# Kernel optimization log

Hardware: AMD Instinct MI355X
Metric: run time of the kernel (lower is better)

## Reference

```python
import jax, jax.numpy as jnp
import numpy as np
import math

N_HEADS = 16
D_KV = 64
NUM_BUCKETS = 32
MAX_DISTANCE = 128


def _rel_bucket(rel_pos, num_buckets=NUM_BUCKETS, max_distance=MAX_DISTANCE):
    # bidirectional=True branch of relative_position_bucket
    n = -rel_pos
    num_buckets //= 2
    ret = (n < 0).astype(jnp.int32) * num_buckets
    n = jnp.abs(n)
    max_exact = num_buckets // 2
    is_small = n < max_exact
    val_large = max_exact + (
        jnp.log(n.astype(jnp.float32) / max_exact)
        / math.log(max_distance / max_exact)
        * (num_buckets - max_exact)
    ).astype(jnp.int32)
    val_large = jnp.minimum(val_large, num_buckets - 1)
    return jnp.where(is_small, n, val_large) + ret


def setup_inputs() -> dict:
    key = jax.random.key(0)
    ks = jax.random.split(key, 6)
    T, D = 2048, 1024
    x = jax.random.normal(ks[0], (T, D), dtype=jnp.float32)
    Wq = jax.random.normal(ks[1], (D, N_HEADS * D_KV), dtype=jnp.float32) * 0.02
    Wk = jax.random.normal(ks[2], (D, N_HEADS * D_KV), dtype=jnp.float32) * 0.02
    Wv = jax.random.normal(ks[3], (D, N_HEADS * D_KV), dtype=jnp.float32) * 0.02
    Wo = jax.random.normal(ks[4], (N_HEADS * D_KV, D), dtype=jnp.float32) * 0.02
    rel_bias_table = jax.random.normal(ks[5], (NUM_BUCKETS, N_HEADS), dtype=jnp.float32) * 0.02
    q_lens = jnp.full((4,), 512, dtype=jnp.int32)  # packed varlen: 4 seqs of 512, sum == T
    return {"x": x, "Wq": Wq, "Wk": Wk, "Wv": Wv, "Wo": Wo,
            "rel_bias_table": rel_bias_table, "q_lens": q_lens}


def _attention(x, Wq, Wk, Wv, Wo, rel_bias_table, q_lens):
    T = x.shape[0]
    q = x @ Wq
    k = x @ Wk
    v = x @ Wv
    to_heads = lambda t: jnp.transpose(t.reshape(T, N_HEADS, D_KV), (1, 0, 2))  # [H,T,d]
    q_h, k_h, v_h = to_heads(q), to_heads(k), to_heads(v)

    # fp32 scores (no 1/sqrt(d) scaling in T5; module uses scaling=1.0)
    scores = jnp.einsum('hqd,hkd->hqk', q_h.astype(jnp.float32), k_h.astype(jnp.float32))

    # sequence ids / positions within packed layout
    starts = jnp.cumsum(q_lens, dtype=jnp.int32) - q_lens
    indicators = jnp.zeros(T, dtype=jnp.int32).at[starts].set(1)
    seq_ids = jnp.cumsum(indicators, dtype=jnp.int32) - 1
    pos = jnp.arange(T) - starts[seq_ids]

    # relative position bias (encoder: bidirectional)
    rel_pos = pos[None, :] - pos[:, None]  # [T,T]
    buckets = _rel_bucket(rel_pos)
    bias = jnp.transpose(rel_bias_table[buckets], (2, 0, 1))  # [H,T,T]
    scores = scores + bias.astype(jnp.float32)

    # block-diagonal mask over packed sequences (non-causal encoder)
    total = jnp.sum(q_lens)
    valid = jnp.arange(T) < total
    mask = (seq_ids[:, None] == seq_ids[None, :]) & valid[:, None] & valid[None, :]
    scores = jnp.where(mask[None], scores, jnp.finfo(scores.dtype).min)

    weights = jax.nn.softmax(scores, axis=-1)
    out = jnp.einsum('hqk,hkd->hqd', weights, v_h.astype(jnp.float32))
    out = jnp.transpose(out, (1, 0, 2)).reshape(T, N_HEADS * D_KV)
    return out.astype(x.dtype) @ Wo


def reference(x, Wq, Wk, Wv, Wo, rel_bias_table, q_lens):
    return _attention(x, Wq, Wk, Wv, Wo, rel_bias_table, q_lens)
```

## Files before the change

### kernel.cpp

```cpp
#include <hip/hip_runtime.h>

#define NH 16

typedef __bf16 bf16x8 __attribute__((ext_vector_type(8)));
typedef unsigned short u16x8 __attribute__((ext_vector_type(8)));
typedef float f32x4 __attribute__((ext_vector_type(4)));
typedef unsigned short u16;

__device__ __forceinline__ u16 f2bu(float f) {
    unsigned int u = __builtin_bit_cast(unsigned int, f);
    u = (u + 0x7FFFu + ((u >> 16) & 1u)) >> 16;
    return (u16)u;
}
__device__ __forceinline__ bf16x8 ld_bf8(const u16* p) {
    return __builtin_bit_cast(bf16x8, *(const u16x8*)p);
}
__device__ __forceinline__ void gl_lds16(const void* g, void* l) {
    __builtin_amdgcn_global_load_lds((const __attribute__((address_space(1))) void*)g,
                                     (__attribute__((address_space(3))) void*)l, 16, 0, 0);
}

__device__ __forceinline__ int rel_bucket(int delta) {
    int n = -delta;
    int ret = (n < 0) ? 16 : 0;
    int na = n < 0 ? -n : n;
    int b;
    if (na < 8) b = na;
    else if (na < 12) b = 8;
    else if (na < 16) b = 9;
    else if (na < 23) b = 10;
    else if (na < 32) b = 11;
    else if (na < 46) b = 12;
    else if (na < 64) b = 13;
    else if (na < 91) b = 14;
    else b = 15;
    return b + ret;
}

#define L2E 1.4426950408889634f

__global__ void prep_all(const float* __restrict__ x, u16* __restrict__ xb, int n,
                         const float* __restrict__ tbl, float* __restrict__ biasT, int T,
                         const int* __restrict__ q_lens, int nseq,
                         int* __restrict__ seqid, int* __restrict__ kvs, int* __restrict__ kve,
                         const float* __restrict__ Wq, const float* __restrict__ Wk,
                         const float* __restrict__ Wv, const float* __restrict__ Wo,
                         u16* __restrict__ Wt, u16* __restrict__ Wot,
                         int cb, int bb, int mb) {
    __shared__ float tile[32][33];
    int b = blockIdx.x, tid = threadIdx.x;
    if (b < cb) {
        int i = (b * 256 + tid) * 4;
        if (i >= n) return;
        float4 v = *(const float4*)&x[i];
        u16 o0 = f2bu(v.x), o1 = f2bu(v.y), o2 = f2bu(v.z), o3 = f2bu(v.w);
        xb[i] = o0; xb[i+1] = o1; xb[i+2] = o2; xb[i+3] = o3;
    } else if (b < cb + bb) {
        int idx = (b - cb) * 256 + tid;
        int W = 2 * T - 1;
        if (idx >= NH * W) return;
        int d = idx % W - (T - 1);
        int h = idx / W;
        biasT[idx] = tbl[rel_bucket(d) * NH + h] * L2E;
    } else if (b < cb + bb + mb) {
        int t = (b - cb - bb) * 256 + tid;
        if (t >= T) return;
        int start = 0, sid = -1, a = 0, e = 0;
        for (int i = 0; i < nseq; ++i) {
            int len = q_lens[i];
            if (t >= start && t < start + len) { sid = i; a = start; e = start + len; }
            start += len;
        }
        seqid[t] = sid; kvs[t] = a; kve[t] = e;
    } else {
        int t = b - cb - bb - mb;
        int z = t >> 10; t &= 1023;
        const float* src = z == 0 ? Wq : z == 1 ? Wk : z == 2 ? Wv : Wo;
        u16* dst = z < 3 ? Wt + (size_t)z * 1024 * 1024 : Wot;
        int r0 = (t >> 5) * 32, c0 = (t & 31) * 32;
        int tx = tid & 31, ty = tid >> 5;
        #pragma unroll
        for (int i = 0; i < 32; i += 8)
            tile[ty + i][tx] = src[(size_t)(r0 + ty + i) * 1024 + c0 + tx];
        __syncthreads();
        #pragma unroll
        for (int i = 0; i < 32; i += 8)
            dst[(size_t)(c0 + ty + i) * 1024 + r0 + tx] = f2bu(tile[tx][ty + i]);
    }
}

template<int MODE, int BM>
__global__ __launch_bounds__(256)
void gemm_bt(const u16* __restrict__ A, const u16* __restrict__ Bt,
             int N, int K, int T,
             float* __restrict__ Cf, u16* __restrict__ qkb, u16* __restrict__ vtb) {
    constexpr int MI = BM / 32;
    constexpr int STG = (BM + 128) * 64;
    constexpr int LDSN = (MODE == 1 && 128 * 136 > 2 * STG) ? 128 * 136 : 2 * STG;
    __shared__ __attribute__((aligned(16))) u16 lds[LDSN];
    const int tid = threadIdx.x;
    const int l = tid & 63, wv = tid >> 6;
    const int l16 = l & 15, lg = l >> 4;
    const int lrow = l >> 3, lslot = l & 7;
    const int wm = (wv >> 1) * (BM / 2), wn = (wv & 1) * 64;

    int nbk = gridDim.x * gridDim.y;
    int lin = blockIdx.y * gridDim.x + blockIdx.x;
    int lin2 = (nbk & 7) ? lin : (lin & 7) * (nbk >> 3) + (lin >> 3);
    const int bm = (lin2 % gridDim.x) * BM;
    const int bn = (lin2 / gridDim.x) * 128;

    f32x4 acc[MI][4];
    #pragma unroll
    for (int i = 0; i < MI; i++)
        #pragma unroll
        for (int j = 0; j < 4; j++)
            #pragma unroll
            for (int r = 0; r < 4; r++) acc[i][j][r] = 0.f;

    auto stage = [&](int k0, int bi) {
        u16* As_ = lds + bi * STG;
        u16* Bs_ = As_ + BM * 64;
        #pragma unroll
        for (int c = 0; c < MI; ++c) {
            int chunk = c * 4 + wv;
            int row = chunk * 8 + lrow;
            int gs = lslot ^ (row & 7);
            gl_lds16(&A[(size_t)(bm + row) * K + k0 + gs * 8], &As_[chunk * 512]);
        }
        #pragma unroll
        for (int c = 0; c < 4; ++c) {
            int chunk = c * 4 + wv;
            int row = chunk * 8 + lrow;
            int gs = lslot ^ (row & 7);
            gl_lds16(&Bt[(size_t)(bn + row) * K + k0 + gs * 8], &Bs_[chunk * 512]);
        }
    };

    stage(0, 0);
    __syncthreads();
    int cur = 0;
    for (int k0 = 0; k0 < K; k0 += 64) {
        if (k0 + 64 < K) stage(k0 + 64, cur ^ 1);
        const u16* As = lds + cur * STG;
        const u16* Bs = As + BM * 64;
        #pragma unroll
        for (int kk = 0; kk < 2; ++kk) {
            bf16x8 af[MI], bfv[4];
            #pragma unroll
            for (int i = 0; i < MI; i++) {
                int row = wm + i * 16 + l16;
                af[i] = ld_bf8(&As[row * 64 + (((kk * 4 + lg) ^ (row & 7)) * 8)]);
            }
            #pragma unroll
            for (int j = 0; j < 4; j++) {
                int row = wn + j * 16 + l16;
                bfv[j] = ld_bf8(&Bs[row * 64 + (((kk * 4 + lg) ^ (row & 7)) * 8)]);
            }
            #pragma unroll
            for (int i = 0; i < MI; i++)
                #pragma unroll
                for (int j = 0; j < 4; j++)
                    acc[i][j] = __builtin_amdgcn_mfma_f32_16x16x32_bf16(af[i], bfv[j], acc[i][j], 0, 0, 0);
        }
        __syncthreads();
        cur ^= 1;
    }

    if (MODE == 0) {
        #pragma unroll
        for (int i = 0; i < MI; i++)
            #pragma unroll
            for (int j = 0; j < 4; j++) {
                int col = bn + wn + j * 16 + l16;
                #pragma unroll
                for (int r = 0; r < 4; r++) {
                    int row = bm + wm + i * 16 + lg * 4 + r;
                    Cf[(size_t)row * N + col] = acc[i][j][r];
                }
            }
    } else if (bn < 2048) {
        #pragma unroll
        for (int i = 0; i < MI; i++)
            #pragma unroll
            for (int j = 0; j < 4; j++) {
                int col = bn + wn + j * 16 + l16;
                #pragma unroll
                for (int r = 0; r < 4; r++) {
                    int row = bm + wm + i * 16 + lg * 4 + r;
                    qkb[(size_t)row * 2048 + col] = f2bu(acc[i][j][r]);
                }
            }
    } else {
        #pragma unroll
        for (int i = 0; i < MI; i++)
            #pragma unroll
            for (int j = 0; j < 4; j++) {
                int cl = wn + j * 16 + l16;
                #pragma unroll
                for (int r = 0; r < 4; r++)
                    ((u16*)lds)[cl * 136 + wm + i * 16 + lg * 4 + r] = f2bu(acc[i][j][r]);
            }
        __syncthreads();
        int cl = tid >> 1, hf = tid & 1;
        size_t gb = (size_t)(bn - 2048 + cl) * T + bm + hf * 64;
        #pragma unroll
        for (int k2 = 0; k2 < 8; ++k2) {
            int4 v4 = *(const int4*)&((u16*)lds)[cl * 136 + hf * 64 + k2 * 8];
            *(int4*)&vtb[gb + k2 * 8] = v4;
        }
    }
}

__global__ __launch_bounds__(256)
void attn_kernel(const u16* __restrict__ qkb, const u16* __restrict__ vtb,
                 const float* __restrict__ biasT,
                 const int* __restrict__ seqid, const int* __restrict__ kvsA,
                 const int* __restrict__ kveA,
                 u16* __restrict__ attnb, int T) {
    __shared__ __attribute__((aligned(16))) u16 KV[2][2][4096];
    __shared__ __attribute__((aligned(16))) u16 Ps[4][16][72];
    __shared__ float biasLds[2304];
    const int tid = threadIdx.x;
    const int l = tid & 63, wv = tid >> 6;
    const int l16 = l & 15, lg = l >> 4;
    const int lrow = l >> 3, lslot = l & 7;
    const int Wb = 2 * T - 1;

    int nbk = gridDim.x * gridDim.y;
    int lin = blockIdx.y * gridDim.x + blockIdx.x;
    int lin2 = (nbk & 7) ? lin : (lin & 7) * (nbk >> 3) + (lin >> 3);
    const int h = lin2 / gridDim.x;
    const int q0 = (lin2 % gridDim.x) * 64;

    bf16x8 qf[2];
    {
        int tq = q0 + wv * 16 + l16;
        const u16* qp = qkb + (size_t)tq * 2048 + h * 64 + lg * 8;
        qf[0] = ld_bf8(qp); qf[1] = ld_bf8(qp + 32);
    }
    const int s0 = seqid[q0], s1 = seqid[q0 + 63];
    const bool uni = (s0 == s1) && (s0 >= 0);
    const int kvA = uni ? kvsA[q0] : 0;
    const int kvB = uni ? kveA[q0] : T;
    const int len = kvB - kvA;

    for (int t = tid; t < len + 126; t += 256) {
        int dlt = kvA - q0 + t - 63;
        dlt = dlt < -(T - 1) ? -(T - 1) : (dlt > T - 1 ? T - 1 : dlt);
        biasLds[t] = biasT[(size_t)h * Wb + dlt + (T - 1)];
    }

    const u16* kg = qkb + 1024 + h * 64;
    const u16* vg = vtb + (size_t)(h * 64) * T;

    auto stage = [&](int base, int bi) {
        #pragma unroll
        for (int c = 0; c < 2; ++c) {
            int chunk = c * 4 + wv;
            int row = chunk * 8 + lrow;
            int gs = lslot ^ (row & 7);
            int tk = base + row; if (tk > T - 1) tk = T - 1;
            gl_lds16(kg + (size_t)tk * 2048 + gs * 8, &KV[bi][0][chunk * 512]);
            gl_lds16(vg + (size_t)row * T + base + gs * 8, &KV[bi][1][chunk * 512]);
        }
    };

    int tqr[4], sqr[4];
    #pragma unroll
    for (int r = 0; r < 4; r++) {
        tqr[r] = q0 + wv * 16 + lg * 4 + r;
        sqr[r] = uni ? s0 : seqid[tqr[r]];
    }
    float psum[4] = {0.f, 0.f, 0.f, 0.f};
    f32x4 o[4];
    #pragma unroll
    for (int d = 0; d < 4; d++)
        #pragma unroll
        for (int r = 0; r < 4; r++) o[d][r] = 0.f;

    stage(kvA, 0);
    __syncthreads();
    int cur = 0;
    for (int base = kvA; base < kvB; base += 64) {
        if (base + 64 < kvB) stage(base + 64, cur ^ 1);
        const u16* Kb = KV[cur][0];
        const u16* Vb = KV[cur][1];

        f32x4 s[4];
        #pragma unroll
        for (int kt = 0; kt < 4; kt++)
            #pragma unroll
            for (int r = 0; r < 4; r++) s[kt][r] = 0.f;
        #pragma unroll
        for (int kk = 0; kk < 2; kk++)
            #pragma unroll
            for (int kt = 0; kt < 4; kt++) {
                int r = kt * 16 + l16;
                bf16x8 kf = ld_bf8(Kb + r * 64 + (((kk * 4 + lg) ^ (r & 7)) * 8));
                s[kt] = __builtin_amdgcn_mfma_f32_16x16x32_bf16(qf[kk], kf, s[kt], 0, 0, 0);
            }

        const bool fullT = (base + 64 <= kvB);
        const int cbi = (base - kvA) + 63 + l16 - wv * 16 - lg * 4;
        #pragma unroll
        for (int r = 0; r < 4; r++) {
            const float* bp = &biasLds[cbi - r];
            #pragma unroll
            for (int kt = 0; kt < 4; kt++) {
                float p = __builtin_amdgcn_exp2f(__builtin_fmaf(s[kt][r], L2E, bp[kt * 16]));
                if (uni) {
                    if (!fullT && base + kt * 16 + l16 >= kvB) p = 0.f;
                } else {
                    int tk = base + kt * 16 + l16;
                    int tkc = tk < T ? tk : T - 1;
                    bool ok = (tk < T) && (seqid[tkc] == sqr[r]);
                    p = (sqr[r] < 0) ? 1.f : (ok ? p : 0.f);
                }
                psum[r] += p;
                Ps[wv][lg * 4 + r][kt * 16 + l16] = f2bu(p);
            }
        }
        bf16x8 pf0 = ld_bf8(&Ps[wv][l16][lg * 8]);
        bf16x8 pf1 = ld_bf8(&Ps[wv][l16][32 + lg * 8]);
        #pragma unroll
        for (int kk = 0; kk < 2; kk++) {
            bf16x8 pf = kk ? pf1 : pf0;
            #pragma unroll
            for (int dt = 0; dt < 4; dt++) {
                int r = dt * 16 + l16;
                bf16x8 vf = ld_bf8(Vb + r * 64 + (((kk * 4 + lg) ^ (r & 7)) * 8));
                o[dt] = __builtin_amdgcn_mfma_f32_16x16x32_bf16(pf, vf, o[dt], 0, 0, 0);
            }
        }
        __syncthreads();
        cur ^= 1;
    }

    float lsum[4];
    #pragma unroll
    for (int r = 0; r < 4; r++) {
        float v = psum[r];
        #pragma unroll
        for (int m = 1; m < 16; m <<= 1) v += __shfl_xor(v, m, 64);
        lsum[r] = v;
    }
    #pragma unroll
    for (int dt = 0; dt < 4; dt++)
        #pragma unroll
        for (int r = 0; r < 4; r++)
            attnb[(size_t)tqr[r] * 1024 + h * 64 + dt * 16 + l16] = f2bu(o[dt][r] / lsum[r]);
}

extern "C" void kernel_launch(void* const* d_in, const int* in_sizes, int n_in,
                              void* d_out, int out_size, void* d_ws, size_t ws_size,
                              hipStream_t stream) {
    const float* x   = (const float*)d_in[0];
    const float* Wq  = (const float*)d_in[1];
    const float* Wk  = (const float*)d_in[2];
    const float* Wv  = (const float*)d_in[3];
    const float* Wo  = (const float*)d_in[4];
    const float* tbl = (const float*)d_in[5];
    const int* q_lens = (const int*)d_in[6];
    const int T = in_sizes[0] / 1024;
    const int nseq = in_sizes[6];

    char* ws = (char*)d_ws;
    auto alloc = [&](size_t bytes) { char* p = ws; ws += (bytes + 255) & ~(size_t)255; return p; };
    u16*   xb    = (u16*)alloc((size_t)T * 1024 * 2);
    u16*   Wt    = (u16*)alloc((size_t)3072 * 1024 * 2);
    u16*   Wot   = (u16*)alloc((size_t)1024 * 1024 * 2);
    u16*   qkb   = (u16*)alloc((size_t)T * 2048 * 2);
    u16*   vtb   = (u16*)alloc((size_t)1024 * T * 2);
    u16*   attnb = (u16*)alloc((size_t)T * 1024 * 2);
    float* biasT = (float*)alloc((size_t)NH * (2 * T - 1) * 4);
    int*   seqid = (int*)alloc((size_t)T * 4);
    int*   kvs   = (int*)alloc((size_t)T * 4);
    int*   kve   = (int*)alloc((size_t)T * 4);

    int cb = (T * 1024 / 4 + 255) / 256;
    int bb = (NH * (2 * T - 1) + 255) / 256;
    int mb = (T + 255) / 256;
    prep_all<<<dim3(cb + bb + mb + 4096), dim3(256), 0, stream>>>(
        x, xb, T * 1024, tbl, biasT, T, q_lens, nseq, seqid, kvs, kve,
        Wq, Wk, Wv, Wo, Wt, Wot, cb, bb, mb);

    gemm_bt<1, 128><<<dim3(T / 128, 3072 / 128), dim3(256), 0, stream>>>(
        xb, Wt, 3072, 1024, T, nullptr, qkb, vtb);
    attn_kernel<<<dim3(T / 64, NH), dim3(256), 0, stream>>>(
        qkb, vtb, biasT, seqid, kvs, kve, attnb, T);
    gemm_bt<0, 64><<<dim3(T / 64, 1024 / 128), dim3(256), 0, stream>>>(
        attnb, Wot, 1024, 1024, T, (float*)d_out, nullptr, nullptr);
}
```

Before: 135.7 us.

## Fuse bias/seqid prep into attention, widen attention tile, XCD-aware GEMM block mapping

```diff
diff --git a/kernel.cpp b/kernel.cpp
--- a/kernel.cpp
+++ b/kernel.cpp
@@ -40,13 +40,9 @@
 #define L2E 1.4426950408889634f
 
 __global__ void prep_all(const float* __restrict__ x, u16* __restrict__ xb, int n,
-                         const float* __restrict__ tbl, float* __restrict__ biasT, int T,
-                         const int* __restrict__ q_lens, int nseq,
-                         int* __restrict__ seqid, int* __restrict__ kvs, int* __restrict__ kve,
                          const float* __restrict__ Wq, const float* __restrict__ Wk,
                          const float* __restrict__ Wv, const float* __restrict__ Wo,
-                         u16* __restrict__ Wt, u16* __restrict__ Wot,
-                         int cb, int bb, int mb) {
+                         u16* __restrict__ Wt, u16* __restrict__ Wot, int cb) {
     __shared__ float tile[32][33];
     int b = blockIdx.x, tid = threadIdx.x;
     if (b < cb) {
@@ -55,25 +51,8 @@
         float4 v = *(const float4*)&x[i];
         u16 o0 = f2bu(v.x), o1 = f2bu(v.y), o2 = f2bu(v.z), o3 = f2bu(v.w);
         xb[i] = o0; xb[i+1] = o1; xb[i+2] = o2; xb[i+3] = o3;
-    } else if (b < cb + bb) {
-        int idx = (b - cb) * 256 + tid;
-        int W = 2 * T - 1;
-        if (idx >= NH * W) return;
-        int d = idx % W - (T - 1);
-        int h = idx / W;
-        biasT[idx] = tbl[rel_bucket(d) * NH + h] * L2E;
-    } else if (b < cb + bb + mb) {
-        int t = (b - cb - bb) * 256 + tid;
-        if (t >= T) return;
-        int start = 0, sid = -1, a = 0, e = 0;
-        for (int i = 0; i < nseq; ++i) {
-            int len = q_lens[i];
-            if (t >= start && t < start + len) { sid = i; a = start; e = start + len; }
-            start += len;
-        }
-        seqid[t] = sid; kvs[t] = a; kve[t] = e;
     } else {
-        int t = b - cb - bb - mb;
+        int t = b - cb;
         int z = t >> 10; t &= 1023;
         const float* src = z == 0 ? Wq : z == 1 ? Wk : z == 2 ? Wv : Wo;
         u16* dst = z < 3 ? Wt + (size_t)z * 1024 * 1024 : Wot;
@@ -89,7 +68,7 @@
     }
 }
 
-template<int MODE, int BM>
+template<int MODE, int BM, int XR, int XC>
 __global__ __launch_bounds__(256)
 void gemm_bt(const u16* __restrict__ A, const u16* __restrict__ Bt,
              int N, int K, int T,
@@ -104,11 +83,19 @@
     const int lrow = l >> 3, lslot = l & 7;
     const int wm = (wv >> 1) * (BM / 2), wn = (wv & 1) * 64;
 
-    int nbk = gridDim.x * gridDim.y;
-    int lin = blockIdx.y * gridDim.x + blockIdx.x;
-    int lin2 = (nbk & 7) ? lin : (lin & 7) * (nbk >> 3) + (lin >> 3);
-    const int bm = (lin2 % gridDim.x) * BM;
-    const int bn = (lin2 / gridDim.x) * 128;
+    int bmi, bni;
+    {
+        int gx = gridDim.x, gy = gridDim.y;
+        int lin = blockIdx.y * gx + blockIdx.x;
+        int nrx = gx / XR, nrc = gy / XC;
+        if (gx % XR == 0 && gy % XC == 0 && nrx * nrc == 8) {
+            int xcd = lin & 7, loc = lin >> 3;
+            int rr = xcd / nrc, rc = xcd % nrc;
+            bmi = rr * XR + (loc % XR);
+            bni = rc * XC + (loc / XR);
+        } else { bmi = blockIdx.x; bni = blockIdx.y; }
+    }
+    const int bm = bmi * BM, bn = bni * 128;
 
     f32x4 acc[MI][4];
     #pragma unroll
@@ -199,39 +186,55 @@
                 int cl = wn + j * 16 + l16;
                 #pragma unroll
                 for (int r = 0; r < 4; r++)
-                    ((u16*)lds)[cl * 136 + wm + i * 16 + lg * 4 + r] = f2bu(acc[i][j][r]);
+                    lds[cl * 136 + wm + i * 16 + lg * 4 + r] = f2bu(acc[i][j][r]);
             }
         __syncthreads();
         int cl = tid >> 1, hf = tid & 1;
         size_t gb = (size_t)(bn - 2048 + cl) * T + bm + hf * 64;
         #pragma unroll
         for (int k2 = 0; k2 < 8; ++k2) {
-            int4 v4 = *(const int4*)&((u16*)lds)[cl * 136 + hf * 64 + k2 * 8];
+            int4 v4 = *(const int4*)&lds[cl * 136 + hf * 64 + k2 * 8];
             *(int4*)&vtb[gb + k2 * 8] = v4;
         }
     }
 }
 
-__global__ __launch_bounds__(256)
+__global__ __launch_bounds__(512)
 void attn_kernel(const u16* __restrict__ qkb, const u16* __restrict__ vtb,
-                 const float* __restrict__ biasT,
-                 const int* __restrict__ seqid, const int* __restrict__ kvsA,
-                 const int* __restrict__ kveA,
+                 const float* __restrict__ tbl, const int* __restrict__ q_lens, int nseq,
                  u16* __restrict__ attnb, int T) {
     __shared__ __attribute__((aligned(16))) u16 KV[2][2][4096];
-    __shared__ __attribute__((aligned(16))) u16 Ps[4][16][72];
+    __shared__ __attribute__((aligned(16))) u16 Ps[8][16][72];
     __shared__ float biasLds[2304];
     const int tid = threadIdx.x;
     const int l = tid & 63, wv = tid >> 6;
     const int l16 = l & 15, lg = l >> 4;
     const int lrow = l >> 3, lslot = l & 7;
-    const int Wb = 2 * T - 1;
 
     int nbk = gridDim.x * gridDim.y;
     int lin = blockIdx.y * gridDim.x + blockIdx.x;
     int lin2 = (nbk & 7) ? lin : (lin & 7) * (nbk >> 3) + (lin >> 3);
     const int h = lin2 / gridDim.x;
-    const int q0 = (lin2 % gridDim.x) * 64;
+    const int q0 = (lin2 % gridDim.x) * 128;
+
+    int cums[9]; cums[0] = 0;
+    #pragma unroll
+    for (int i = 0; i < 8; ++i) cums[i + 1] = cums[i] + (i < nseq ? q_lens[i] : 0);
+    auto seq_of = [&](int t) -> int {
+        int s = -1;
+        #pragma unroll
+        for (int i = 0; i < 8; ++i)
+            if (t >= cums[i] && t < cums[i + 1]) s = i;
+        return s;
+    };
+    const int s0 = seq_of(q0), s1 = seq_of(q0 + 127);
+    const bool uni = (s0 == s1) && (s0 >= 0);
+    const int kvA = uni ? cums[s0] : 0;
+    const int kvB = uni ? cums[s0 + 1] : T;
+    const int len = kvB - kvA;
+
+    for (int t = tid; t < len + 128; t += 512)
+        biasLds[t] = tbl[rel_bucket(kvA - q0 - 127 + t) * NH + h] * L2E;
 
     bf16x8 qf[2];
     {
@@ -239,39 +242,23 @@
         const u16* qp = qkb + (size_t)tq * 2048 + h * 64 + lg * 8;
         qf[0] = ld_bf8(qp); qf[1] = ld_bf8(qp + 32);
     }
-    const int s0 = seqid[q0], s1 = seqid[q0 + 63];
-    const bool uni = (s0 == s1) && (s0 >= 0);
-    const int kvA = uni ? kvsA[q0] : 0;
-    const int kvB = uni ? kveA[q0] : T;
-    const int len = kvB - kvA;
-
-    for (int t = tid; t < len + 126; t += 256) {
-        int dlt = kvA - q0 + t - 63;
-        dlt = dlt < -(T - 1) ? -(T - 1) : (dlt > T - 1 ? T - 1 : dlt);
-        biasLds[t] = biasT[(size_t)h * Wb + dlt + (T - 1)];
+    int tqr[4], sqr[4];
+    #pragma unroll
+    for (int r = 0; r < 4; r++) {
+        tqr[r] = q0 + wv * 16 + lg * 4 + r;
+        sqr[r] = uni ? s0 : seq_of(tqr[r]);
     }
 
     const u16* kg = qkb + 1024 + h * 64;
     const u16* vg = vtb + (size_t)(h * 64) * T;
-
     auto stage = [&](int base, int bi) {
-        #pragma unroll
-        for (int c = 0; c < 2; ++c) {
-            int chunk = c * 4 + wv;
-            int row = chunk * 8 + lrow;
-            int gs = lslot ^ (row & 7);
-            int tk = base + row; if (tk > T - 1) tk = T - 1;
-            gl_lds16(kg + (size_t)tk * 2048 + gs * 8, &KV[bi][0][chunk * 512]);
-            gl_lds16(vg + (size_t)row * T + base + gs * 8, &KV[bi][1][chunk * 512]);
-        }
+        int row = wv * 8 + lrow;
+        int gs = lslot ^ (row & 7);
+        int tk = base + row; if (tk > T - 1) tk = T - 1;
+        gl_lds16(kg + (size_t)tk * 2048 + gs * 8, &KV[bi][0][wv * 512]);
+        gl_lds16(vg + (size_t)row * T + base + gs * 8, &KV[bi][1][wv * 512]);
     };
 
-    int tqr[4], sqr[4];
-    #pragma unroll
-    for (int r = 0; r < 4; r++) {
-        tqr[r] = q0 + wv * 16 + lg * 4 + r;
-        sqr[r] = uni ? s0 : seqid[tqr[r]];
-    }
     float psum[4] = {0.f, 0.f, 0.f, 0.f};
     f32x4 o[4];
     #pragma unroll
@@ -296,29 +283,46 @@
         for (int kk = 0; kk < 2; kk++)
             #pragma unroll
             for (int kt = 0; kt < 4; kt++) {
-                int r = kt * 16 + l16;
-                bf16x8 kf = ld_bf8(Kb + r * 64 + (((kk * 4 + lg) ^ (r & 7)) * 8));
+                int rw = kt * 16 + l16;
+                bf16x8 kf = ld_bf8(Kb + rw * 64 + (((kk * 4 + lg) ^ (rw & 7)) * 8));
                 s[kt] = __builtin_amdgcn_mfma_f32_16x16x32_bf16(qf[kk], kf, s[kt], 0, 0, 0);
             }
 
-        const bool fullT = (base + 64 <= kvB);
-        const int cbi = (base - kvA) + 63 + l16 - wv * 16 - lg * 4;
-        #pragma unroll
-        for (int r = 0; r < 4; r++) {
-            const float* bp = &biasLds[cbi - r];
+        const int cbi = (base - kvA) + 127 + l16 - wv * 16 - lg * 4;
+        if (uni && base + 64 <= kvB) {
+            #pragma unroll
+            for (int r = 0; r < 4; r++) {
+                const float* bp = &biasLds[cbi - r];
+                #pragma unroll
+                for (int kt = 0; kt < 4; kt++) {
+                    float p = __builtin_amdgcn_exp2f(__builtin_fmaf(s[kt][r], L2E, bp[kt * 16]));
+                    psum[r] += p;
+                    Ps[wv][lg * 4 + r][kt * 16 + l16] = f2bu(p);
+                }
+            }
+        } else {
+            int skt[4];
             #pragma unroll
             for (int kt = 0; kt < 4; kt++) {
-                float p = __builtin_amdgcn_exp2f(__builtin_fmaf(s[kt][r], L2E, bp[kt * 16]));
-                if (uni) {
-                    if (!fullT && base + kt * 16 + l16 >= kvB) p = 0.f;
-                } else {
-                    int tk = base + kt * 16 + l16;
-                    int tkc = tk < T ? tk : T - 1;
-                    bool ok = (tk < T) && (seqid[tkc] == sqr[r]);
-                    p = (sqr[r] < 0) ? 1.f : (ok ? p : 0.f);
+                int tk = base + kt * 16 + l16;
+                skt[kt] = (tk < T) ? (uni ? s0 : seq_of(tk)) : -2;
+            }
+            #pragma unroll
+            for (int r = 0; r < 4; r++) {
+                const float* bp = &biasLds[cbi - r];
+                #pragma unroll
+                for (int kt = 0; kt < 4; kt++) {
+                    float p = __builtin_amdgcn_exp2f(__builtin_fmaf(s[kt][r], L2E, bp[kt * 16]));
+                    if (uni) {
+                        int tk = base + kt * 16 + l16;
+                        if (tk >= kvB) p = 0.f;
+                    } else {
+                        bool ok = (skt[kt] >= 0) && (skt[kt] == sqr[r]);
+                        p = (sqr[r] < 0) ? 1.f : (ok ? p : 0.f);
+                    }
+                    psum[r] += p;
+                    Ps[wv][lg * 4 + r][kt * 16 + l16] = f2bu(p);
                 }
-                psum[r] += p;
-                Ps[wv][lg * 4 + r][kt * 16 + l16] = f2bu(p);
             }
         }
         bf16x8 pf0 = ld_bf8(&Ps[wv][l16][lg * 8]);
@@ -328,8 +332,8 @@
             bf16x8 pf = kk ? pf1 : pf0;
             #pragma unroll
             for (int dt = 0; dt < 4; dt++) {
-                int r = dt * 16 + l16;
-                bf16x8 vf = ld_bf8(Vb + r * 64 + (((kk * 4 + lg) ^ (r & 7)) * 8));
+                int rw = dt * 16 + l16;
+                bf16x8 vf = ld_bf8(Vb + rw * 64 + (((kk * 4 + lg) ^ (rw & 7)) * 8));
                 o[dt] = __builtin_amdgcn_mfma_f32_16x16x32_bf16(pf, vf, o[dt], 0, 0, 0);
             }
         }
@@ -373,22 +377,15 @@
     u16*   qkb   = (u16*)alloc((size_t)T * 2048 * 2);
     u16*   vtb   = (u16*)alloc((size_t)1024 * T * 2);
     u16*   attnb = (u16*)alloc((size_t)T * 1024 * 2);
-    float* biasT = (float*)alloc((size_t)NH * (2 * T - 1) * 4);
-    int*   seqid = (int*)alloc((size_t)T * 4);
-    int*   kvs   = (int*)alloc((size_t)T * 4);
-    int*   kve   = (int*)alloc((size_t)T * 4);
 
     int cb = (T * 1024 / 4 + 255) / 256;
-    int bb = (NH * (2 * T - 1) + 255) / 256;
-    int mb = (T + 255) / 256;
-    prep_all<<<dim3(cb + bb + mb + 4096), dim3(256), 0, stream>>>(
-        x, xb, T * 1024, tbl, biasT, T, q_lens, nseq, seqid, kvs, kve,
-        Wq, Wk, Wv, Wo, Wt, Wot, cb, bb, mb);
-
-    gemm_bt<1, 128><<<dim3(T / 128, 3072 / 128), dim3(256), 0, stream>>>(
+    prep_all<<<dim3(cb + 4096), dim3(256), 0, stream>>>(
+        x, xb, T * 1024, Wq, Wk, Wv, Wo, Wt, Wot, cb);
+
+    gemm_bt<1, 128, 8, 6><<<dim3(T / 128, 3072 / 128), dim3(256), 0, stream>>>(
         xb, Wt, 3072, 1024, T, nullptr, qkb, vtb);
-    attn_kernel<<<dim3(T / 64, NH), dim3(256), 0, stream>>>(
-        qkb, vtb, biasT, seqid, kvs, kve, attnb, T);
-    gemm_bt<0, 64><<<dim3(T / 64, 1024 / 128), dim3(256), 0, stream>>>(
+    attn_kernel<<<dim3(T / 128, NH), dim3(512), 0, stream>>>(
+        qkb, vtb, tbl, q_lens, nseq, attnb, T);
+    gemm_bt<0, 64, 8, 4><<<dim3(T / 64, 1024 / 128), dim3(256), 0, stream>>>(
         attnb, Wot, 1024, 1024, T, (float*)d_out, nullptr, nullptr);
 }
```

New measurement: 129.0 us. -4.9%, faster.
